# Kernel optimization log

Hardware: AMD Instinct MI355X
Metric: run time of the kernel (lower is better)

The kernel has to match this reference:

```python
import jax, jax.numpy as jnp
import numpy as np

N, E, C, S = 10000, 100000, 64, 10      # nodes, edges, channels, species
NB, H = 8, 64                            # num_bessel, radial-MLP hidden
R_MAX = 5.0
AVG_NEIGH = 10.0
# irrep degree l for each of the 16 spherical-harmonic components (l_max=3)
L_IDX = np.array([0] + [1]*3 + [2]*5 + [3]*7)


def _sph(u):
    # real spherical harmonics up to l=3 on unit vectors u: [E,3] -> [E,16]
    x, y, z = u[:, 0], u[:, 1], u[:, 2]
    s3, s5, s15 = jnp.sqrt(3.0), jnp.sqrt(5.0), jnp.sqrt(15.0)
    a, b = jnp.sqrt(35.0 / 8.0), jnp.sqrt(21.0 / 8.0)
    s105, s7 = jnp.sqrt(105.0), jnp.sqrt(7.0)
    return jnp.stack([
        jnp.ones_like(x),
        s3 * x, s3 * y, s3 * z,
        s15 * x * y, s15 * y * z, 0.5 * s5 * (3 * z * z - 1.0),
        s15 * x * z, 0.5 * s15 * (x * x - y * y),
        a * y * (3 * x * x - y * y), s105 * x * y * z, b * y * (5 * z * z - 1.0),
        0.5 * s7 * z * (5 * z * z - 3.0), b * x * (5 * z * z - 1.0),
        0.5 * s105 * z * (x * x - y * y), a * x * (x * x - 3 * y * y),
    ], axis=-1)


def _bessel(r):
    # Bessel radial basis with smooth polynomial envelope (RadialEmbeddingLayer)
    u = r / R_MAX
    k = jnp.arange(1, NB + 1, dtype=r.dtype)
    env = jnp.where(u < 1.0, (1.0 - u) ** 2 * (1.0 + 2.0 * u), 0.0)
    return jnp.sqrt(2.0 / R_MAX) * jnp.sin(k * jnp.pi * u[:, None]) / r[:, None] * env[:, None]


def setup_inputs() -> dict:
    key = jax.random.key(0)
    ks = jax.random.split(key, 20)
    f = lambda k, s: jax.random.normal(k, s, dtype=jnp.float32)
    return {
        "edge_vectors": f(ks[0], (E, 3)),
        "node_species": jax.random.randint(ks[1], (N,), 0, S),
        "senders": jax.random.randint(ks[2], (E,), 0, N),
        "receivers": jax.random.randint(ks[3], (E,), 0, N),
        "node_embed_W": f(ks[4], (S, C)) * 0.5,
        "l1_lin_up": f(ks[5], (C, C)) / jnp.sqrt(1.0 * C),
        "l1_rW1": f(ks[6], (NB, H)) / jnp.sqrt(1.0 * NB),
        "l1_rW2": f(ks[7], (H, C * 4)) * (0.1 / jnp.sqrt(1.0 * H)),
        "l1_sel_W": f(ks[8], (S, C, C)) / jnp.sqrt(1.0 * C),
        "l1_pw": f(ks[9], (S, 3, C)) * 0.5,
        "l1_uw": f(ks[10], (S, 3, C)) * 0.5,
        "l1_ro_w": f(ks[11], (C,)) / jnp.sqrt(1.0 * C),
        "l2_lin_up": f(ks[12], (C, C)) / jnp.sqrt(1.0 * C),
        "l2_rW1": f(ks[13], (NB, H)) / jnp.sqrt(1.0 * NB),
        "l2_rW2": f(ks[14], (H, C * 4)) * (0.1 / jnp.sqrt(1.0 * H)),
        "l2_res_W": f(ks[15], (S, C, C)) / jnp.sqrt(1.0 * C),
        "l2_pw": f(ks[16], (S, 3, C)) * 0.5,
        "l2_ro_W1": f(ks[17], (C, 16)) / jnp.sqrt(1.0 * C),
        "l2_ro_W2": f(ks[18], (16,)) * 0.25,
    }


def reference(edge_vectors, node_species, senders, receivers, node_embed_W,
              l1_lin_up, l1_rW1, l1_rW2, l1_sel_W, l1_pw, l1_uw, l1_ro_w,
              l2_lin_up, l2_rW1, l2_rW2, l2_res_W, l2_pw, l2_ro_W1, l2_ro_W2):
    n = node_species.shape[0]
    r = jnp.sqrt(jnp.sum(edge_vectors ** 2, axis=-1) + 1e-12)  # safe_norm
    u = edge_vectors / r[:, None]
    sh = _sph(u)                  # [E,16]
    radial = _bessel(r)           # [E,NB]

    # LinearNodeEmbeddingLayer: species -> C scalar channels
    x0 = node_embed_W[node_species]                              # [N,C]

    # ---- layer 1: interaction (selector TP variant), not last ----
    h1 = x0 @ l1_lin_up                                          # [N,C]
    rw1 = jax.nn.silu(radial @ l1_rW1) @ l1_rW2                  # [E,C*4]
    rw1 = rw1.reshape(-1, C, 4)[:, :, L_IDX]                     # [E,C,16] per-l radial weight
    msg1 = rw1 * sh[:, None, :] * h1[senders][:, :, None]        # [E,C,16] edge tensor product
    agg1 = jax.ops.segment_sum(msg1, receivers, num_segments=n) / AVG_NEIGH  # [N,C,16]

    # selector TP: species-indexed channel mixing
    feats = jnp.einsum('ncd,ndk->nck', l1_sel_W[node_species], agg1)
    s, v = feats[:, :, 0], feats[:, :, 1:4]
    # equivariant product basis, correlation=3, target 0e+1o per channel
    pw, uw = l1_pw[node_species], l1_uw[node_species]            # [N,3,C]
    out0 = pw[:, 0] * s + pw[:, 1] * s * s + pw[:, 2] * s * s * s       # [N,C] scalars
    outv = (uw[:, 0] + uw[:, 1] * s + uw[:, 2] * s * s)[:, :, None] * v  # [N,C,3] vectors
    ro1 = out0 @ l1_ro_w                                          # linear readout [N]

    # ---- layer 2: interaction (residual variant), last -> scalars ----
    h2 = out0 @ l2_lin_up                                         # [N,C]
    # 1o x 1o -> 0e path: sender vector dotted with edge direction
    edge_dot = jnp.einsum('eck,ek->ec', outv[senders], u)         # [E,C]
    rw2 = jax.nn.silu(radial @ l2_rW1) @ l2_rW2
    rw2 = rw2.reshape(-1, C, 4)[:, :, L_IDX]                      # [E,C,16]
    msg2 = rw2 * sh[:, None, :] * (h2[senders] + edge_dot)[:, :, None]
    agg2 = jax.ops.segment_sum(msg2, receivers, num_segments=n) / AVG_NEIGH

    res = jnp.einsum('ncd,nd->nc', l2_res_W[node_species], out0)  # residual FCTP with species 0e
    s2 = agg2[:, :, 0]
    p2 = l2_pw[node_species]
    out2 = p2[:, 0] * s2 + p2[:, 1] * s2 * s2 + p2[:, 2] * s2 * s2 * s2 + res
    ro2 = jax.nn.silu(out2 @ l2_ro_W1) @ l2_ro_W2                 # nonlinear readout [N]

    # e3nn.stack over layers and heads: [N, num_interactions, num_heads, 0e]
    return jnp.stack([ro1, ro2], axis=1)[:, :, None, None]
```

## Files before the change

### kernel.cpp

```cpp
#include <hip/hip_runtime.h>
#include <hip/hip_bf16.h>
#include <math.h>

#define N_NODES 10000
#define N_EDGES 100000
#define NCH 64
#define NSPEC 10

typedef __attribute__((ext_vector_type(8))) short short8v;
typedef __attribute__((ext_vector_type(4))) float f32x4;

static __device__ __forceinline__ unsigned short f2bf(float f){
  unsigned u = __float_as_uint(f);
  u += 0x7fff + ((u >> 16) & 1);
  return (unsigned short)(u >> 16);
}
static __device__ __forceinline__ float bf2f(unsigned u){
  return __uint_as_float(u << 16);
}
static __device__ __forceinline__ unsigned packbf(float a, float b){
  return (unsigned)f2bf(a) | ((unsigned)f2bf(b) << 16);
}

__global__ void k_count(const int* __restrict__ recv, int* __restrict__ cnt){
  int i = blockIdx.x*blockDim.x + threadIdx.x;
  if (i < N_EDGES) atomicAdd(&cnt[recv[i]], 1);
}

__global__ __launch_bounds__(256) void k_pre(
  int* __restrict__ cursor,
  const float* __restrict__ sel, const float* __restrict__ resw,
  float* __restrict__ selT, float* __restrict__ resT,
  const int* __restrict__ species, const float* __restrict__ embedW,
  const float* __restrict__ linup, unsigned short* __restrict__ h1p,
  const float* __restrict__ rW2a, const float* __restrict__ rW2b,
  unsigned short* __restrict__ wfrag)
{
  int b = blockIdx.x;
  int tid = threadIdx.x;
  if (b < 40){
    int i = b*256 + tid;
    if (i < N_NODES) cursor[i] = 0;
  } else if (b < 200){
    int i = (b-40)*256 + tid;
    int s = i >> 12, r = i & 4095, d = r >> 6, c = r & 63;
    int src = s*4096 + c*64 + d;
    selT[i] = sel[src];
    resT[i] = resw[src];
  } else if (b < 2700){
    int w = ((b-200)*256 + tid) >> 6;
    int lane = tid & 63;
    int sp = __builtin_amdgcn_readfirstlane(species[w]);
    const float* x0 = embedW + sp*NCH;
    float acc = 0.f;
    #pragma unroll
    for (int d = 0; d < NCH; d++) acc += x0[d] * linup[d*NCH + lane];
    h1p[w*NCH + lane] = f2bf(acc);
  } else {
    int i = (b-2700)*256 + tid;
    int slot = i >> 9;
    int rem  = i & 511;
    int lane = rem >> 3, j = rem & 7;
    int cl = lane & 15, hb = (lane >> 4)*8;
    float v;
    if (slot < 16){
      int t = slot >> 2, f = slot & 3;
      int colofs = f >> 1, off = (f & 1)*32;
      v = rW2a[(hb + off + j)*256 + 4*(t*16 + cl) + colofs];
    } else {
      int s2 = slot - 16;
      int t = s2 >> 1, f = s2 & 1;
      int off = f*32;
      v = rW2b[(hb + off + j)*256 + 4*(t*16 + cl)];
    }
    wfrag[i] = f2bf(v);
  }
}

__global__ __launch_bounds__(256) void k_scanrw(
    int* __restrict__ cnt_cursor, int* __restrict__ starts,
    const float* __restrict__ ev,
    const float* __restrict__ rW1a, const float* __restrict__ rW1b,
    const unsigned short* __restrict__ wfrag,
    unsigned* __restrict__ rw12p, unsigned short* __restrict__ rwBp,
    float4* __restrict__ shu)
{
  __shared__ short s_hid1[64*72];
  __shared__ short s_hid2[64*72];

  int tid = threadIdx.x;

  if (blockIdx.x == 0){
    int* stot = (int*)s_hid1;
    int base = tid*40;
    int loc[40];
    int sum = 0;
    #pragma unroll
    for (int j = 0; j < 40; j++){
      int i = base + j;
      int v = (i < N_NODES) ? cnt_cursor[i] : 0;
      loc[j] = sum; sum += v;
    }
    stot[tid] = sum;
    __syncthreads();
    for (int off = 1; off < 256; off <<= 1){
      int t = (tid >= off) ? stot[tid-off] : 0;
      __syncthreads();
      stot[tid] += t;
      __syncthreads();
    }
    int excl = stot[tid] - sum;
    #pragma unroll
    for (int j = 0; j < 40; j++){
      int i = base + j;
      if (i < N_NODES){ int st = excl + loc[j]; starts[i] = st; cnt_cursor[i] = st; }
    }
    if (tid == 255) starts[N_NODES] = stot[255];
    return;
  }

  int e0 = (blockIdx.x-1)*64;
  int lane = tid & 63;
  int w = __builtin_amdgcn_readfirstlane(tid >> 6);

  int e = e0 + lane;
  bool act = (e < N_EDGES);
  float ex = 0.f, ey = 0.f, ez = 1.f;
  if (act){ ex = ev[e*3+0]; ey = ev[e*3+1]; ez = ev[e*3+2]; }
  float r = sqrtf(ex*ex + ey*ey + ez*ez + 1e-12f);
  float rinv = 1.0f / r;
  float u = r * 0.2f;
  float env = 0.f;
  if (u < 1.f){ float om = 1.f - u; env = om*om*(1.f + 2.f*u); }
  float pref = 0.6324555320336759f * rinv * env;
  float rad[8];
  #pragma unroll
  for (int b = 0; b < 8; b++)
    rad[b] = pref * __sinf((float)(b+1) * 3.14159265358979f * u);
  if (w == 0 && act) shu[e] = make_float4(ex*rinv, ey*rinv, ez*rinv, 0.f);

  {
    short8v hv0, hv1, gv0, gv1;
    #pragma unroll
    for (int j = 0; j < 16; j++){
      int h = w*16 + j;
      float a1 = 0.f, a2 = 0.f;
      #pragma unroll
      for (int b = 0; b < 8; b++){
        a1 += rad[b] * rW1a[b*64 + h];
        a2 += rad[b] * rW1b[b*64 + h];
      }
      float hd1 = a1 / (1.f + __expf(-a1));
      float hd2 = a2 / (1.f + __expf(-a2));
      unsigned short q1 = f2bf(hd1), q2 = f2bf(hd2);
      if (j < 8){ hv0[j] = (short)q1; gv0[j] = (short)q2; }
      else      { hv1[j-8] = (short)q1; gv1[j-8] = (short)q2; }
    }
    *(short8v*)&s_hid1[lane*72 + w*16]     = hv0;
    *(short8v*)&s_hid1[lane*72 + w*16 + 8] = hv1;
    *(short8v*)&s_hid2[lane*72 + w*16]     = gv0;
    *(short8v*)&s_hid2[lane*72 + w*16 + 8] = gv1;
  }
  __syncthreads();

  int cl = lane & 15;
  int hb = (lane >> 4) * 8;
  int rowq = (lane >> 4) * 4;

  short8v a0  = *(short8v*)&s_hid1[(w*16 + cl)*72 + hb];
  short8v a1  = *(short8v*)&s_hid1[(w*16 + cl)*72 + hb + 32];
  short8v c0f = *(short8v*)&s_hid2[(w*16 + cl)*72 + hb];
  short8v c1f = *(short8v*)&s_hid2[(w*16 + cl)*72 + hb + 32];

  const short8v* wf1 = (const short8v*)wfrag;
  const short8v* wf2 = ((const short8v*)wfrag) + 1024;

  f32x4 ax[4], ay[4], bc[4];
  #pragma unroll
  for (int t = 0; t < 4; t++){
    ax[t] = (f32x4)(0.f); ay[t] = (f32x4)(0.f); bc[t] = (f32x4)(0.f);
  }
  #pragma unroll
  for (int t = 0; t < 4; t++){
    short8v bx0 = wf1[(t*4+0)*64 + lane];
    short8v bx1 = wf1[(t*4+1)*64 + lane];
    short8v by0 = wf1[(t*4+2)*64 + lane];
    short8v by1 = wf1[(t*4+3)*64 + lane];
    short8v b20 = wf2[(t*2+0)*64 + lane];
    short8v b21 = wf2[(t*2+1)*64 + lane];
    ax[t] = __builtin_amdgcn_mfma_f32_16x16x32_bf16(a0, bx0, ax[t], 0, 0, 0);
    ax[t] = __builtin_amdgcn_mfma_f32_16x16x32_bf16(a1, bx1, ax[t], 0, 0, 0);
    ay[t] = __builtin_amdgcn_mfma_f32_16x16x32_bf16(a0, by0, ay[t], 0, 0, 0);
    ay[t] = __builtin_amdgcn_mfma_f32_16x16x32_bf16(a1, by1, ay[t], 0, 0, 0);
    bc[t] = __builtin_amdgcn_mfma_f32_16x16x32_bf16(c0f, b20, bc[t], 0, 0, 0);
    bc[t] = __builtin_amdgcn_mfma_f32_16x16x32_bf16(c1f, b21, bc[t], 0, 0, 0);
  }
  #pragma unroll
  for (int t = 0; t < 4; t++){
    #pragma unroll
    for (int i = 0; i < 4; i++){
      int er = e0 + w*16 + rowq + i;
      if (er < N_EDGES){
        rw12p[(size_t)er*64 + t*16 + cl] = packbf(ax[t][i], ay[t][i]);
        rwBp [(size_t)er*64 + t*16 + cl] = f2bf(bc[t][i]);
      }
    }
  }
}

__global__ void k_fill(const int* __restrict__ recv, int* __restrict__ cursor, int* __restrict__ elist){
  int i = blockIdx.x*blockDim.x + threadIdx.x;
  if (i < N_EDGES){ int pos = atomicAdd(&cursor[recv[i]], 1); elist[pos] = i; }
}

__global__ __launch_bounds__(256) void k_node1(
  const int* __restrict__ senders, const int* __restrict__ species,
  const int* __restrict__ starts, const int* __restrict__ elist,
  const float4* __restrict__ shu,
  const unsigned* __restrict__ rw12p, const unsigned short* __restrict__ h1p,
  const float* __restrict__ selT,
  const float* __restrict__ pw, const float* __restrict__ uwv,
  const float* __restrict__ row,
  const float* __restrict__ linup2, const float* __restrict__ resT,
  float* __restrict__ out,
  uint2* __restrict__ outvp, float* __restrict__ reso)
{
  int lane  = threadIdx.x & 63;
  int wslot = threadIdx.x >> 6;
  int n = blockIdx.x*4 + wslot;
  __shared__ float4 sacc[4][64];

  int s0 = __builtin_amdgcn_readfirstlane(starts[n]);
  int s1 = __builtin_amdgcn_readfirstlane(starts[n+1]);
  int sp = __builtin_amdgcn_readfirstlane(species[n]);

  float acc0 = 0.f, acc1 = 0.f, acc2 = 0.f, acc3 = 0.f;
  for (int base = s0; base < s1; base += 64){
    int m = min(64, s1 - base);
    int e_l = 0, snd_l = 0;
    if (lane < m){
      e_l   = elist[base + lane];
      snd_l = senders[e_l];
    }
    for (int t = 0; t < m; t += 4){
      int i0 = t;
      int i1 = min(t+1, m-1), i2 = min(t+2, m-1), i3 = min(t+3, m-1);
      float w1 = (t+1 < m) ? 1.f : 0.f;
      float w2 = (t+2 < m) ? 1.f : 0.f;
      float w3 = (t+3 < m) ? 1.f : 0.f;
      int e0i = __builtin_amdgcn_readfirstlane(__shfl(e_l, i0, 64));
      int s0i = __builtin_amdgcn_readfirstlane(__shfl(snd_l, i0, 64));
      int e1i = __builtin_amdgcn_readfirstlane(__shfl(e_l, i1, 64));
      int s1i = __builtin_amdgcn_readfirstlane(__shfl(snd_l, i1, 64));
      int e2i = __builtin_amdgcn_readfirstlane(__shfl(e_l, i2, 64));
      int s2i = __builtin_amdgcn_readfirstlane(__shfl(snd_l, i2, 64));
      int e3i = __builtin_amdgcn_readfirstlane(__shfl(e_l, i3, 64));
      int s3i = __builtin_amdgcn_readfirstlane(__shfl(snd_l, i3, 64));
      unsigned p0 = rw12p[(size_t)e0i*64 + lane];
      unsigned p1 = rw12p[(size_t)e1i*64 + lane];
      unsigned p2 = rw12p[(size_t)e2i*64 + lane];
      unsigned p3 = rw12p[(size_t)e3i*64 + lane];
      float h0 = bf2f(h1p[s0i*64 + lane]);
      float h1v = bf2f(h1p[s1i*64 + lane]) * w1;
      float h2v = bf2f(h1p[s2i*64 + lane]) * w2;
      float h3v = bf2f(h1p[s3i*64 + lane]) * w3;
      float4 v0 = shu[e0i];
      float4 v1 = shu[e1i];
      float4 v2 = shu[e2i];
      float4 v3 = shu[e3i];
      acc0 += bf2f(p0 & 0xffffu)*h0;  float m0 = bf2f(p0 >> 16)*h0;
      acc1 += m0*v0.x; acc2 += m0*v0.y; acc3 += m0*v0.z;
      acc0 += bf2f(p1 & 0xffffu)*h1v; float m1 = bf2f(p1 >> 16)*h1v;
      acc1 += m1*v1.x; acc2 += m1*v1.y; acc3 += m1*v1.z;
      acc0 += bf2f(p2 & 0xffffu)*h2v; float m2 = bf2f(p2 >> 16)*h2v;
      acc1 += m2*v2.x; acc2 += m2*v2.y; acc3 += m2*v2.z;
      acc0 += bf2f(p3 & 0xffffu)*h3v; float m3 = bf2f(p3 >> 16)*h3v;
      acc1 += m3*v3.x; acc2 += m3*v3.y; acc3 += m3*v3.z;
    }
  }
  const float c10 = 0.1f;
  const float c13 = 0.17320508075688773f;
  sacc[wslot][lane] = make_float4(acc0*c10, acc1*c13, acc2*c13, acc3*c13);
  asm volatile("s_waitcnt lgkmcnt(0)" ::: "memory");

  const float* selp = selT + sp*4096;
  float f0 = 0.f, f1 = 0.f, f2 = 0.f, f3 = 0.f;
  #pragma unroll 8
  for (int d = 0; d < 64; d++){
    float wv = selp[d*64 + lane];
    float4 a = sacc[wslot][d];
    f0 += wv*a.x; f1 += wv*a.y; f2 += wv*a.z; f3 += wv*a.w;
  }

  float s = f0;
  const float* pwp = pw  + sp*192;
  const float* uwp = uwv + sp*192;
  float pw0 = pwp[lane], pw1 = pwp[64+lane], pw2 = pwp[128+lane];
  float uw0 = uwp[lane], uw1 = uwp[64+lane], uw2 = uwp[128+lane];
  float ss = s*s;
  float o0  = pw0*s + pw1*ss + pw2*ss*s;
  float uco = uw0 + uw1*s + uw2*ss;

  float rv = o0 * row[lane];
  #pragma unroll
  for (int off = 32; off >= 1; off >>= 1) rv += __shfl_xor(rv, off, 64);
  if (lane == 0) out[n*2 + 0] = rv;

  float* so = reinterpret_cast<float*>(&sacc[wslot][0]);
  asm volatile("s_waitcnt lgkmcnt(0)" ::: "memory");
  so[lane] = o0;
  asm volatile("s_waitcnt lgkmcnt(0)" ::: "memory");

  float hh = 0.f, rr = 0.f;
  const float* resp = resT + sp*4096;
  #pragma unroll 8
  for (int d = 0; d < 64; d++){
    float od = so[d];
    hh += od * linup2[d*64 + lane];
    rr += od * resp[d*64 + lane];
  }
  uint2 op;
  op.x = packbf(uco*f1, uco*f2);
  op.y = packbf(uco*f3, hh);
  outvp[n*64 + lane] = op;
  reso[n*64 + lane] = rr;
}

__global__ __launch_bounds__(256) void k_node2(
  const int* __restrict__ senders, const int* __restrict__ species,
  const int* __restrict__ starts, const int* __restrict__ elist,
  const float4* __restrict__ shu,
  const unsigned short* __restrict__ rwBp,
  const uint2* __restrict__ outvp, const float* __restrict__ reso,
  const float* __restrict__ pw2,
  const float* __restrict__ roW1, const float* __restrict__ roW2,
  float* __restrict__ out)
{
  int lane  = threadIdx.x & 63;
  int wslot = threadIdx.x >> 6;
  int n = blockIdx.x*4 + wslot;
  __shared__ float sout[4][64];

  int s0 = __builtin_amdgcn_readfirstlane(starts[n]);
  int s1 = __builtin_amdgcn_readfirstlane(starts[n+1]);
  int sp = __builtin_amdgcn_readfirstlane(species[n]);

  float acc = 0.f;
  for (int base = s0; base < s1; base += 64){
    int m = min(64, s1 - base);
    int e_l = 0, snd_l = 0;
    if (lane < m){
      e_l   = elist[base + lane];
      snd_l = senders[e_l];
    }
    for (int t = 0; t < m; t += 4){
      int i0 = t;
      int i1 = min(t+1, m-1), i2 = min(t+2, m-1), i3 = min(t+3, m-1);
      float w1 = (t+1 < m) ? 1.f : 0.f;
      float w2 = (t+2 < m) ? 1.f : 0.f;
      float w3 = (t+3 < m) ? 1.f : 0.f;
      int e0i = __builtin_amdgcn_readfirstlane(__shfl(e_l, i0, 64));
      int s0i = __builtin_amdgcn_readfirstlane(__shfl(snd_l, i0, 64));
      int e1i = __builtin_amdgcn_readfirstlane(__shfl(e_l, i1, 64));
      int s1i = __builtin_amdgcn_readfirstlane(__shfl(snd_l, i1, 64));
      int e2i = __builtin_amdgcn_readfirstlane(__shfl(e_l, i2, 64));
      int s2i = __builtin_amdgcn_readfirstlane(__shfl(snd_l, i2, 64));
      int e3i = __builtin_amdgcn_readfirstlane(__shfl(e_l, i3, 64));
      int s3i = __builtin_amdgcn_readfirstlane(__shfl(snd_l, i3, 64));
      float r0 = bf2f(rwBp[(size_t)e0i*64 + lane]);
      float r1 = bf2f(rwBp[(size_t)e1i*64 + lane]) * w1;
      float r2 = bf2f(rwBp[(size_t)e2i*64 + lane]) * w2;
      float r3 = bf2f(rwBp[(size_t)e3i*64 + lane]) * w3;
      uint2 o0v = outvp[s0i*64 + lane];
      uint2 o1v = outvp[s1i*64 + lane];
      uint2 o2v = outvp[s2i*64 + lane];
      uint2 o3v = outvp[s3i*64 + lane];
      float4 v0 = shu[e0i];
      float4 v1 = shu[e1i];
      float4 v2 = shu[e2i];
      float4 v3 = shu[e3i];
      acc += r0 * (bf2f(o0v.y >> 16) + bf2f(o0v.x & 0xffffu)*v0.x
                   + bf2f(o0v.x >> 16)*v0.y + bf2f(o0v.y & 0xffffu)*v0.z);
      acc += r1 * (bf2f(o1v.y >> 16) + bf2f(o1v.x & 0xffffu)*v1.x
                   + bf2f(o1v.x >> 16)*v1.y + bf2f(o1v.y & 0xffffu)*v1.z);
      acc += r2 * (bf2f(o2v.y >> 16) + bf2f(o2v.x & 0xffffu)*v2.x
                   + bf2f(o2v.x >> 16)*v2.y + bf2f(o2v.y & 0xffffu)*v2.z);
      acc += r3 * (bf2f(o3v.y >> 16) + bf2f(o3v.x & 0xffffu)*v3.x
                   + bf2f(o3v.x >> 16)*v3.y + bf2f(o3v.y & 0xffffu)*v3.z);
    }
  }
  float s2 = acc * 0.1f;
  const float* p2 = pw2 + sp*192;
  float q0 = p2[lane], q1 = p2[64+lane], q2 = p2[128+lane];
  float s2s = s2*s2;
  float o2 = q0*s2 + q1*s2s + q2*s2s*s2 + reso[n*64 + lane];

  sout[wslot][lane] = o2;
  asm volatile("s_waitcnt lgkmcnt(0)" ::: "memory");

  int j = lane & 15, g = lane >> 4;
  float qp = 0.f;
  #pragma unroll
  for (int t = 0; t < 16; t++){
    int c = g*16 + t;
    qp += sout[wslot][c] * roW1[c*16 + j];
  }
  qp += __shfl_xor(qp, 16, 64);
  qp += __shfl_xor(qp, 32, 64);
  float sil = qp / (1.f + __expf(-qp));
  float contrib = sil * roW2[j];
  contrib += __shfl_xor(contrib, 1, 64);
  contrib += __shfl_xor(contrib, 2, 64);
  contrib += __shfl_xor(contrib, 4, 64);
  contrib += __shfl_xor(contrib, 8, 64);
  if (lane == 0) out[n*2 + 1] = contrib;
}

extern "C" void kernel_launch(void* const* d_in, const int* in_sizes, int n_in,
                              void* d_out, int out_size, void* d_ws, size_t ws_size,
                              hipStream_t stream)
{
  const float* ev     = (const float*)d_in[0];
  const int*   spec   = (const int*)  d_in[1];
  const int*   send   = (const int*)  d_in[2];
  const int*   recv   = (const int*)  d_in[3];
  const float* embedW = (const float*)d_in[4];
  const float* l1_lin = (const float*)d_in[5];
  const float* l1_rW1 = (const float*)d_in[6];
  const float* l1_rW2 = (const float*)d_in[7];
  const float* l1_sel = (const float*)d_in[8];
  const float* l1_pw  = (const float*)d_in[9];
  const float* l1_uw  = (const float*)d_in[10];
  const float* l1_row = (const float*)d_in[11];
  const float* l2_lin = (const float*)d_in[12];
  const float* l2_rW1 = (const float*)d_in[13];
  const float* l2_rW2 = (const float*)d_in[14];
  const float* l2_res = (const float*)d_in[15];
  const float* l2_pw  = (const float*)d_in[16];
  const float* l2_roW1= (const float*)d_in[17];
  const float* l2_roW2= (const float*)d_in[18];
  float* out = (float*)d_out;

  char* w = (char*)d_ws;
  unsigned*       rw12p = (unsigned*)w;       w += (size_t)N_EDGES*64*4;
  unsigned short* rwBp  = (unsigned short*)w; w += (size_t)N_EDGES*64*2;
  unsigned short* h1p   = (unsigned short*)w; w += (size_t)N_NODES*64*2;
  uint2*  outvp = (uint2*)w;  w += (size_t)N_NODES*64*8;
  float*  reso  = (float*)w;  w += (size_t)N_NODES*64*4;
  float*  selT  = (float*)w;  w += (size_t)NSPEC*4096*4;
  float*  resT  = (float*)w;  w += (size_t)NSPEC*4096*4;
  float4* shu   = (float4*)w; w += (size_t)N_EDGES*16;
  unsigned short* wfrag = (unsigned short*)w; w += 12288*2;
  int* starts = (int*)w;      w += (size_t)(N_NODES+1)*4;
  int* cursor = (int*)w;      w += (size_t)N_NODES*4;
  int* elist  = (int*)w;      w += (size_t)N_EDGES*4;

  k_pre  <<<2748, 256, 0, stream>>>(cursor, l1_sel, l2_res, selT, resT,
                                    spec, embedW, l1_lin, h1p,
                                    l1_rW2, l2_rW2, wfrag);
  k_count<<<(N_EDGES+255)/256, 256, 0, stream>>>(recv, cursor);
  k_scanrw<<<1 + (N_EDGES+63)/64, 256, 0, stream>>>(cursor, starts,
        ev, l1_rW1, l2_rW1, wfrag, rw12p, rwBp, shu);
  k_fill <<<(N_EDGES+255)/256, 256, 0, stream>>>(recv, cursor, elist);
  k_node1<<<N_NODES/4, 256, 0, stream>>>(send, spec, starts, elist, shu, rw12p, h1p,
        selT, l1_pw, l1_uw, l1_row, l2_lin, resT, out, outvp, reso);
  k_node2<<<N_NODES/4, 256, 0, stream>>>(send, spec, starts, elist, shu, rwBp,
        outvp, reso, l2_pw, l2_roW1, l2_roW2, out);
}
```

Before: 92.31 us.

## Process nodes in species-sorted order to improve per-species weight cache locality

Adds a counting sort of nodes by species, with its counting, prefix and scatter steps folded into the existing count, scan and fill kernels. The node kernels then map each wavefront to a node taken from the sorted list, so neighbouring waves share the same per-species weight matrices (selT, resT). This is meant to cut cache misses on the 16 KB per-species matrices. The cost is extra atomics, a serial species scan, and scattered writes to the output and node buffers.

```diff
diff --git a/kernel.cpp b/kernel.cpp
--- a/kernel.cpp
+++ b/kernel.cpp
@@ -6,6 +6,8 @@
 #define N_EDGES 100000
 #define NCH 64
 #define NSPEC 10
+#define EBLK 391
+#define NBLK 40
 
 typedef __attribute__((ext_vector_type(8))) short short8v;
 typedef __attribute__((ext_vector_type(4))) float f32x4;
@@ -22,13 +24,20 @@
   return (unsigned)f2bf(a) | ((unsigned)f2bf(b) << 16);
 }
 
-__global__ void k_count(const int* __restrict__ recv, int* __restrict__ cnt){
-  int i = blockIdx.x*blockDim.x + threadIdx.x;
-  if (i < N_EDGES) atomicAdd(&cnt[recv[i]], 1);
+__global__ void k_count(const int* __restrict__ recv, int* __restrict__ cnt,
+                        const int* __restrict__ species, int* __restrict__ spcnt){
+  int b = blockIdx.x;
+  if (b < EBLK){
+    int i = b*blockDim.x + threadIdx.x;
+    if (i < N_EDGES) atomicAdd(&cnt[recv[i]], 1);
+  } else {
+    int j = (b-EBLK)*blockDim.x + threadIdx.x;
+    if (j < N_NODES) atomicAdd(&spcnt[species[j]], 1);
+  }
 }
 
 __global__ __launch_bounds__(256) void k_pre(
-  int* __restrict__ cursor,
+  int* __restrict__ cursor, int* __restrict__ spcnt, int* __restrict__ spcur,
   const float* __restrict__ sel, const float* __restrict__ resw,
   float* __restrict__ selT, float* __restrict__ resT,
   const int* __restrict__ species, const float* __restrict__ embedW,
@@ -41,6 +50,7 @@
   if (b < 40){
     int i = b*256 + tid;
     if (i < N_NODES) cursor[i] = 0;
+    if (b == 0 && tid < NSPEC){ spcnt[tid] = 0; spcur[tid] = 0; }
   } else if (b < 200){
     int i = (b-40)*256 + tid;
     int s = i >> 12, r = i & 4095, d = r >> 6, c = r & 63;
@@ -79,6 +89,7 @@
 
 __global__ __launch_bounds__(256) void k_scanrw(
     int* __restrict__ cnt_cursor, int* __restrict__ starts,
+    int* __restrict__ spcnt, int* __restrict__ spcur,
     const float* __restrict__ ev,
     const float* __restrict__ rW1a, const float* __restrict__ rW1b,
     const unsigned short* __restrict__ wfrag,
@@ -116,6 +127,11 @@
       if (i < N_NODES){ int st = excl + loc[j]; starts[i] = st; cnt_cursor[i] = st; }
     }
     if (tid == 255) starts[N_NODES] = stot[255];
+    if (tid == 0){
+      int run = 0;
+      #pragma unroll
+      for (int s = 0; s < NSPEC; s++){ int c = spcnt[s]; spcur[s] = run; run += c; }
+    }
     return;
   }
 
@@ -208,14 +224,24 @@
   }
 }
 
-__global__ void k_fill(const int* __restrict__ recv, int* __restrict__ cursor, int* __restrict__ elist){
-  int i = blockIdx.x*blockDim.x + threadIdx.x;
-  if (i < N_EDGES){ int pos = atomicAdd(&cursor[recv[i]], 1); elist[pos] = i; }
+__global__ void k_fill(const int* __restrict__ recv, int* __restrict__ cursor,
+                       int* __restrict__ elist,
+                       const int* __restrict__ species, int* __restrict__ spcur,
+                       int* __restrict__ nsort){
+  int b = blockIdx.x;
+  if (b < EBLK){
+    int i = b*blockDim.x + threadIdx.x;
+    if (i < N_EDGES){ int pos = atomicAdd(&cursor[recv[i]], 1); elist[pos] = i; }
+  } else {
+    int j = (b-EBLK)*blockDim.x + threadIdx.x;
+    if (j < N_NODES){ int pos = atomicAdd(&spcur[species[j]], 1); nsort[pos] = j; }
+  }
 }
 
 __global__ __launch_bounds__(256) void k_node1(
   const int* __restrict__ senders, const int* __restrict__ species,
   const int* __restrict__ starts, const int* __restrict__ elist,
+  const int* __restrict__ nsort,
   const float4* __restrict__ shu,
   const unsigned* __restrict__ rw12p, const unsigned short* __restrict__ h1p,
   const float* __restrict__ selT,
@@ -227,7 +253,7 @@
 {
   int lane  = threadIdx.x & 63;
   int wslot = threadIdx.x >> 6;
-  int n = blockIdx.x*4 + wslot;
+  int n = __builtin_amdgcn_readfirstlane(nsort[blockIdx.x*4 + wslot]);
   __shared__ float4 sacc[4][64];
 
   int s0 = __builtin_amdgcn_readfirstlane(starts[n]);
@@ -329,6 +355,7 @@
 __global__ __launch_bounds__(256) void k_node2(
   const int* __restrict__ senders, const int* __restrict__ species,
   const int* __restrict__ starts, const int* __restrict__ elist,
+  const int* __restrict__ nsort,
   const float4* __restrict__ shu,
   const unsigned short* __restrict__ rwBp,
   const uint2* __restrict__ outvp, const float* __restrict__ reso,
@@ -338,7 +365,7 @@
 {
   int lane  = threadIdx.x & 63;
   int wslot = threadIdx.x >> 6;
-  int n = blockIdx.x*4 + wslot;
+  int n = __builtin_amdgcn_readfirstlane(nsort[blockIdx.x*4 + wslot]);
   __shared__ float sout[4][64];
 
   int s0 = __builtin_amdgcn_readfirstlane(starts[n]);
@@ -454,16 +481,19 @@
   int* starts = (int*)w;      w += (size_t)(N_NODES+1)*4;
   int* cursor = (int*)w;      w += (size_t)N_NODES*4;
   int* elist  = (int*)w;      w += (size_t)N_EDGES*4;
-
-  k_pre  <<<2748, 256, 0, stream>>>(cursor, l1_sel, l2_res, selT, resT,
+  int* nsort  = (int*)w;      w += (size_t)N_NODES*4;
+  int* spcnt  = (int*)w;      w += 16*4;
+  int* spcur  = (int*)w;      w += 16*4;
+
+  k_pre  <<<2748, 256, 0, stream>>>(cursor, spcnt, spcur, l1_sel, l2_res, selT, resT,
                                     spec, embedW, l1_lin, h1p,
                                     l1_rW2, l2_rW2, wfrag);
-  k_count<<<(N_EDGES+255)/256, 256, 0, stream>>>(recv, cursor);
-  k_scanrw<<<1 + (N_EDGES+63)/64, 256, 0, stream>>>(cursor, starts,
+  k_count<<<EBLK + NBLK, 256, 0, stream>>>(recv, cursor, spec, spcnt);
+  k_scanrw<<<1 + (N_EDGES+63)/64, 256, 0, stream>>>(cursor, starts, spcnt, spcur,
         ev, l1_rW1, l2_rW1, wfrag, rw12p, rwBp, shu);
-  k_fill <<<(N_EDGES+255)/256, 256, 0, stream>>>(recv, cursor, elist);
-  k_node1<<<N_NODES/4, 256, 0, stream>>>(send, spec, starts, elist, shu, rw12p, h1p,
+  k_fill <<<EBLK + NBLK, 256, 0, stream>>>(recv, cursor, elist, spec, spcur, nsort);
+  k_node1<<<N_NODES/4, 256, 0, stream>>>(send, spec, starts, elist, nsort, shu, rw12p, h1p,
         selT, l1_pw, l1_uw, l1_row, l2_lin, resT, out, outvp, reso);
-  k_node2<<<N_NODES/4, 256, 0, stream>>>(send, spec, starts, elist, shu, rwBp,
+  k_node2<<<N_NODES/4, 256, 0, stream>>>(send, spec, starts, elist, nsort, shu, rwBp,
         outvp, reso, l2_pw, l2_roW1, l2_roW2, out);
 }
```

New measurement: 152.5 us. +65.2%, slower.
